# Performance work log

Hardware: AMD Instinct MI355X
Metric: run time of the kernel (lower is better)

Reference implementation:

```python
import jax, jax.numpy as jnp
import numpy as np

B, T, C = 2, 2048, 1024
H = 16
HD = C // H  # 64
SCALE = 0.1 / (HD ** 0.5)


def setup_inputs() -> dict:
    key = jax.random.key(0)
    k1, k2, k3 = jax.random.split(key, 3)
    x = jax.random.normal(k1, (B, T, C), dtype=jnp.float32)
    W_attn = jax.random.normal(k2, (C, 3 * C), dtype=jnp.float32) * (C ** -0.5)
    b_attn = jnp.zeros((3 * C,), dtype=jnp.float32)
    W_proj = jax.random.normal(k3, (C, C), dtype=jnp.float32) * (C ** -0.5)
    b_proj = jnp.zeros((C,), dtype=jnp.float32)
    return {"x": x, "W_attn": W_attn, "b_attn": b_attn, "W_proj": W_proj, "b_proj": b_proj}


def reference(x, W_attn, b_attn, W_proj, b_proj):
    Bx, Tx, Cx = x.shape
    qkv = x @ W_attn + b_attn  # [B,T,3C]
    q, k, v = jnp.split(qkv, 3, axis=-1)
    # [B,T,C] -> [B,H,T,HD]
    q = q.reshape(Bx, Tx, H, HD).transpose(0, 2, 1, 3)
    k = k.reshape(Bx, Tx, H, HD).transpose(0, 2, 1, 3)
    v = v.reshape(Bx, Tx, H, HD).transpose(0, 2, 1, 3)
    # note the extra 0.1 factor baked into this module's scaling
    attn = jnp.einsum('bhqd,bhkd->bhqk', q, k) * SCALE
    causal = jnp.tril(jnp.ones((Tx, Tx), dtype=bool))
    attn = jnp.where(causal[None, None, :, :], attn, -jnp.inf)
    attn = jax.nn.softmax(attn, axis=-1)
    y = jnp.einsum('bhqk,bhkd->bhqd', attn, v)
    y = y.transpose(0, 2, 1, 3).reshape(Bx, Tx, Cx)
    return y @ W_proj + b_proj
```

## Files before the change

kernel.cpp:

```cpp
#include <hip/hip_runtime.h>

typedef unsigned short u16;
typedef unsigned int u32;
typedef float f32x4 __attribute__((ext_vector_type(4)));
typedef float f32x16 __attribute__((ext_vector_type(16)));
typedef __bf16 bf16x8 __attribute__((ext_vector_type(8)));
typedef u16 u16x8 __attribute__((ext_vector_type(8)));
typedef u32 u32x4 __attribute__((ext_vector_type(4)));

#define ATT_SCALE 0.0125f
#define LOG2E 1.4426950408889634f

__device__ __forceinline__ u16 f2bf(float x) {
  unsigned u = __builtin_bit_cast(unsigned, x);
  u += 0x7fffu + ((u >> 16) & 1u);
  return (u16)(u >> 16);
}

__device__ __forceinline__ u32 pack_bf16(float lo, float hi) {
  __bf16 a = (__bf16)lo, b = (__bf16)hi;
  return ((u32)__builtin_bit_cast(u16, b) << 16) | __builtin_bit_cast(u16, a);
}

__device__ __forceinline__ float fexp2(float x) {
  return __builtin_amdgcn_exp2f(x);
}

__device__ __forceinline__ f32x4 mfma16(u16x8 a, u16x8 b, f32x4 c) {
  return __builtin_amdgcn_mfma_f32_16x16x32_bf16(
      __builtin_bit_cast(bf16x8, a), __builtin_bit_cast(bf16x8, b), c, 0, 0, 0);
}

__device__ __forceinline__ f32x16 mfma32(u16x8 a, u16x8 b, f32x16 c) {
  return __builtin_amdgcn_mfma_f32_32x32x16_bf16(
      __builtin_bit_cast(bf16x8, a), __builtin_bit_cast(bf16x8, b), c, 0, 0, 0);
}

__device__ __forceinline__ void gl_lds16(const void* g, void* l) {
  __builtin_amdgcn_global_load_lds(
      (__attribute__((address_space(1))) void*)g,
      (__attribute__((address_space(3))) void*)l, 16, 0, 0);
}

__global__ void k_pre(const float* __restrict__ x, const float* __restrict__ W_attn,
                      const float* __restrict__ W_proj, u16* __restrict__ x_bf,
                      u16* __restrict__ Wt_a, u16* __restrict__ Wt_p) {
  __shared__ float tile[32][33];
  const int id = blockIdx.x, tid = threadIdx.x;
  if (id < 2048) {
    int base = id * 2048 + tid * 4;
#pragma unroll
    for (int s = 0; s < 2; ++s) {
      int i = base + s * 1024;
      float4 v = *(const float4*)&x[i];
      ushort4 o;
      o.x = f2bf(v.x); o.y = f2bf(v.y); o.z = f2bf(v.z); o.w = f2bf(v.w);
      *(ushort4*)&x_bf[i] = o;
    }
    return;
  }
  const float* in;
  u16* outp;
  int rows, cols, bx, by;
  if (id < 5120) {
    int t2 = id - 2048;
    bx = t2 % 96; by = t2 / 96;
    in = W_attn; outp = Wt_a; rows = 1024; cols = 3072;
  } else {
    int t3 = id - 5120;
    bx = t3 & 31; by = t3 >> 5;
    in = W_proj; outp = Wt_p; rows = 1024; cols = 1024;
  }
  int tx = tid & 31, ty = tid >> 5;
  int n0 = bx * 32, k0 = by * 32;
#pragma unroll
  for (int i = 0; i < 32; i += 8)
    tile[ty + i][tx] = in[(size_t)(k0 + ty + i) * cols + n0 + tx];
  __syncthreads();
#pragma unroll
  for (int i = 0; i < 32; i += 8)
    outp[(size_t)(n0 + ty + i) * rows + k0 + tx] = f2bf(tile[tx][ty + i]);
}

__global__ void k_gemm_qkv(const u16* __restrict__ A, const u16* __restrict__ Bt,
                           const float* __restrict__ bias,
                           u16* __restrict__ qb, u16* __restrict__ kb, u16* __restrict__ vTb) {
  __shared__ u16 Al[128 * 64];
  __shared__ u16 Bl[128 * 64];
  const int tid = threadIdx.x;
  const int lane = tid & 63;
  const int w = tid >> 6;
  const int m0 = blockIdx.y * 128;
  const int n0 = blockIdx.x * 128;
  const int wr = (w >> 1) * 64;
  const int wc = (w & 1) * 64;
  const int lr = lane & 15;
  const int lk = (lane >> 4) * 8;

  f32x4 acc[4][4] = {};

  for (int k0 = 0; k0 < 1024; k0 += 64) {
#pragma unroll
    for (int it = 0; it < 4; ++it) {
      int off = (it * 256 + tid) * 8;
      int r = off >> 6, c = off & 63;
      gl_lds16(&A[(size_t)(m0 + r) * 1024 + k0 + c], &Al[off]);
      gl_lds16(&Bt[(size_t)(n0 + r) * 1024 + k0 + c], &Bl[off]);
    }
    __syncthreads();
#pragma unroll
    for (int kk = 0; kk < 64; kk += 32) {
      u16x8 af[4], bf[4];
#pragma unroll
      for (int i = 0; i < 4; ++i) {
        af[i] = *(const u16x8*)&Al[(wr + i * 16 + lr) * 64 + kk + lk];
        bf[i] = *(const u16x8*)&Bl[(wc + i * 16 + lr) * 64 + kk + lk];
      }
#pragma unroll
      for (int i = 0; i < 4; ++i)
#pragma unroll
        for (int j = 0; j < 4; ++j)
          acc[i][j] = mfma16(af[i], bf[j], acc[i][j]);
    }
    __syncthreads();
  }

#pragma unroll
  for (int i = 0; i < 4; ++i) {
    int rowb = m0 + wr + i * 16 + ((lane >> 4) << 2);
#pragma unroll
    for (int j = 0; j < 4; ++j) {
      int col = n0 + wc + j * 16 + lr;
      float bv = bias[col];
      int which = col >> 10;
      int c = col & 1023;
      int h = c >> 6, d = c & 63;
      int b_ = rowb >> 11, t0 = rowb & 2047;
      int bh = b_ * 16 + h;
      if (which == 2) {
        ushort4 st;
        st.x = f2bf(acc[i][j][0] + bv);
        st.y = f2bf(acc[i][j][1] + bv);
        st.z = f2bf(acc[i][j][2] + bv);
        st.w = f2bf(acc[i][j][3] + bv);
        *(ushort4*)&vTb[((size_t)bh * 64 + d) * 2048 + t0] = st;
      } else {
        u16* dst = (which == 0) ? qb : kb;
        float sc = (which == 0) ? (ATT_SCALE * LOG2E) : 1.0f;
#pragma unroll
        for (int r = 0; r < 4; ++r) {
          float fv = (acc[i][j][r] + bv) * sc;
          dst[((size_t)bh * 2048 + t0 + r) * 64 + d] = f2bf(fv);
        }
      }
    }
  }
}

__device__ __forceinline__ void stage_pair(const u16* __restrict__ kb_bh,
                                           const u16* __restrict__ vT_bh,
                                           u16* Kd, u16* Vd, int kv0, int tid) {
#pragma unroll
  for (int it = 0; it < 4; ++it) {
    int ch = it * 256 + tid;
    int r = ch >> 3, c = ch & 7;
    gl_lds16(&kb_bh[(size_t)(kv0 + r) * 64 + (c ^ (r & 7)) * 8], &Kd[ch * 8]);
    int r2 = ch >> 4, c2 = ch & 15;
    int h2 = c2 >> 3, cc = c2 & 7;
    gl_lds16(&vT_bh[(size_t)r2 * 2048 + kv0 + (h2 * 8 + (cc ^ (r2 & 7))) * 8],
             &Vd[ch * 8]);
  }
}

__global__ __launch_bounds__(256) void k_attn(const u16* __restrict__ qb,
                                              const u16* __restrict__ kb,
                                              const u16* __restrict__ vTb,
                                              u16* __restrict__ yb) {
  __shared__ u16 Kl[2][8192];
  __shared__ u16 Vl[2][8192];

  const int tid = threadIdx.x, lane = tid & 63, w = tid >> 6;
  const int wq = w & 1;
  const int wp = w >> 1;
  const int id = blockIdx.x;
  const int bh = (id & 7) + ((id >> 7) << 3);
  const int pairi = (id >> 3) & 15;
  const int b_ = bh >> 4, h = bh & 15;
  const int ql = lane & 31;
  const int hi = lane >> 5;

  const u16* kb_bh = kb + (size_t)bh * 2048 * 64;
  const u16* vT_bh = vTb + (size_t)bh * 64 * 2048;

#pragma unroll 1
  for (int phase = 0; phase < 2; ++phase) {
    const int qt = phase ? (31 - pairi) : pairi;
    const int q0w = qt * 64 + wq * 32;
    const int qg = q0w + ql;
    const int lim = wq * 32 + ql;

    const u16* qrow = qb + ((size_t)bh * 2048 + qg) * 64;
    u16x8 qf[4];
#pragma unroll
    for (int ks = 0; ks < 4; ++ks)
      qf[ks] = *(const u16x8*)&qrow[ks * 16 + hi * 8];

    f32x16 o0 = {}, o1 = {};
    float mrow = -1e30f, lrow = 0.f;

    const int nkv = qt + 1;
    const int niter = (nkv + 1) >> 1;
    stage_pair(kb_bh, vT_bh, Kl[0], Vl[0], 0, tid);
    int cur = 0;

#pragma unroll 1
    for (int it = 0; it < niter; ++it) {
      if (it + 1 < niter) {
        stage_pair(kb_bh, vT_bh, Kl[cur ^ 1], Vl[cur ^ 1], (it + 1) * 128, tid);
        asm volatile("s_waitcnt vmcnt(8)" ::: "memory");
      } else {
        asm volatile("s_waitcnt vmcnt(0)" ::: "memory");
      }
      __builtin_amdgcn_sched_barrier(0);
      __builtin_amdgcn_s_barrier();

      const int mytile = 2 * it + wp;
      if (mytile <= qt) {
        const u16* Kc = Kl[cur];
        const u16* Vc = Vl[cur];
        const int rbase = wp * 64;

        f32x16 s0 = {}, s1 = {};
        __builtin_amdgcn_s_setprio(1);
#pragma unroll
        for (int ks = 0; ks < 4; ++ks) {
          int ch = 2 * ks + hi;
          int r0 = rbase + ql, r1 = rbase + 32 + ql;
          u16x8 kf0 = *(const u16x8*)&Kc[r0 * 64 + ((ch ^ (r0 & 7)) * 8)];
          u16x8 kf1 = *(const u16x8*)&Kc[r1 * 64 + ((ch ^ (r1 & 7)) * 8)];
          s0 = mfma32(kf0, qf[ks], s0);
          s1 = mfma32(kf1, qf[ks], s1);
        }
        __builtin_amdgcn_s_setprio(0);

        const bool diag = (mytile == qt);
        float pv[32];
        float tmax = -1e30f;
#pragma unroll
        for (int r = 0; r < 16; ++r) {
          float a = s0[r], b2 = s1[r];
          if (diag) {
            int kl0 = (r & 3) + 8 * (r >> 2) + 4 * hi;
            if (kl0 > lim) a = -1e30f;
            if (kl0 + 32 > lim) b2 = -1e30f;
          }
          pv[r] = a;
          pv[16 + r] = b2;
          tmax = fmaxf(tmax, fmaxf(a, b2));
        }
        float rmax = fmaxf(tmax, __shfl_xor(tmax, 32, 64));

        if (__any(rmax > mrow + 8.0f)) {
          float mn = fmaxf(mrow, rmax);
          float al = fexp2(mrow - mn);
          mrow = mn;
          lrow *= al;
#pragma unroll
          for (int r = 0; r < 16; ++r) { o0[r] *= al; o1[r] *= al; }
        }

        u32 pw[16];
#pragma unroll
        for (int j = 0; j < 16; ++j) {
          float e0 = fexp2(pv[2 * j] - mrow);
          float e1 = fexp2(pv[2 * j + 1] - mrow);
          lrow += e0 + e1;
          pw[j] = pack_bf16(e0, e1);
        }

#pragma unroll
        for (int tt = 0; tt < 2; ++tt)
#pragma unroll
          for (int u = 0; u < 2; ++u)
#pragma unroll
            for (int z = 0; z < 2; ++z) {
              int jA = tt * 8 + u * 4 + z;
              asm volatile("v_permlane32_swap_b32 %0, %1"
                           : "+v"(pw[jA]), "+v"(pw[jA + 2]));
            }

        __builtin_amdgcn_s_setprio(1);
#pragma unroll
        for (int ks = 0; ks < 4; ++ks) {
          u32x4 pwv = {pw[4 * ks], pw[4 * ks + 1], pw[4 * ks + 2], pw[4 * ks + 3]};
          u16x8 pfrag = __builtin_bit_cast(u16x8, pwv);
          int ch = 2 * ks + hi;
          int rv0 = ql, rv1 = 32 + ql;
          u16x8 vf0 = *(const u16x8*)&Vc[rv0 * 128 + (wp * 8 + (ch ^ (rv0 & 7))) * 8];
          u16x8 vf1 = *(const u16x8*)&Vc[rv1 * 128 + (wp * 8 + (ch ^ (rv1 & 7))) * 8];
          o0 = mfma32(vf0, pfrag, o0);
          o1 = mfma32(vf1, pfrag, o1);
        }
        __builtin_amdgcn_s_setprio(0);
      }
      __builtin_amdgcn_s_barrier();
      cur ^= 1;
    }

    __syncthreads();
    float* mb = (float*)&Kl[0][0];
    if (wp == 1) {
      float4* dst = (float4*)&mb[(wq * 64 + lane) * 37];
      float4 hd; hd.x = mrow; hd.y = lrow; hd.z = 0.f; hd.w = 0.f;
      dst[0] = hd;
#pragma unroll
      for (int j = 0; j < 4; ++j) {
        float4 t0 = {o0[4 * j], o0[4 * j + 1], o0[4 * j + 2], o0[4 * j + 3]};
        float4 t1 = {o1[4 * j], o1[4 * j + 1], o1[4 * j + 2], o1[4 * j + 3]};
        dst[1 + j] = t0;
        dst[5 + j] = t1;
      }
    }
    __syncthreads();
    if (wp == 0) {
      const float4* src = (const float4*)&mb[(wq * 64 + lane) * 37];
      float4 hd = src[0];
      float m2 = hd.x, l2 = hd.y;
      float m = fmaxf(mrow, m2);
      float a1 = fexp2(mrow - m), a2 = fexp2(m2 - m);
      float l = lrow * a1 + l2 * a2;
      l += __shfl_xor(l, 32, 64);
      float inv = 1.0f / l;

      size_t ybase = ((size_t)b_ * 2048 + qg) * 1024 + h * 64;
#pragma unroll
      for (int dt = 0; dt < 2; ++dt) {
#pragma unroll
        for (int rg = 0; rg < 4; ++rg) {
          float4 po = src[1 + dt * 4 + rg];
          const f32x16& ov = dt ? o1 : o0;
          int d0 = dt * 32 + 8 * rg + 4 * hi;
          ushort4 st;
          st.x = f2bf((ov[rg * 4 + 0] * a1 + po.x * a2) * inv);
          st.y = f2bf((ov[rg * 4 + 1] * a1 + po.y * a2) * inv);
          st.z = f2bf((ov[rg * 4 + 2] * a1 + po.z * a2) * inv);
          st.w = f2bf((ov[rg * 4 + 3] * a1 + po.w * a2) * inv);
          *(ushort4*)&yb[ybase + d0] = st;
        }
      }
    }
    __syncthreads();
  }
}

__global__ void k_gemm_out(const u16* __restrict__ A, const u16* __restrict__ Bt,
                           const float* __restrict__ bias, float* __restrict__ out) {
  __shared__ u16 Al[64 * 64];
  __shared__ u16 Bl[128 * 64];
  const int tid = threadIdx.x;
  const int lane = tid & 63;
  const int w = tid >> 6;
  const int m0 = blockIdx.y * 64;
  const int n0 = blockIdx.x * 128;
  const int wr = (w >> 1) * 32;
  const int wc = (w & 1) * 64;
  const int lr = lane & 15;
  const int lk = (lane >> 4) * 8;

  f32x4 acc[2][4] = {};

  for (int k0 = 0; k0 < 1024; k0 += 64) {
#pragma unroll
    for (int it = 0; it < 2; ++it) {
      int ch = it * 256 + tid;
      int r = ch >> 3, c = (ch & 7) * 8;
      gl_lds16(&A[(size_t)(m0 + r) * 1024 + k0 + c], &Al[ch * 8]);
    }
#pragma unroll
    for (int it = 0; it < 4; ++it) {
      int ch = it * 256 + tid;
      int r = ch >> 3, c = (ch & 7) * 8;
      gl_lds16(&Bt[(size_t)(n0 + r) * 1024 + k0 + c], &Bl[ch * 8]);
    }
    __syncthreads();
#pragma unroll
    for (int kk = 0; kk < 64; kk += 32) {
      u16x8 af[2], bf[4];
#pragma unroll
      for (int i = 0; i < 2; ++i)
        af[i] = *(const u16x8*)&Al[(wr + i * 16 + lr) * 64 + kk + lk];
#pragma unroll
      for (int j = 0; j < 4; ++j)
        bf[j] = *(const u16x8*)&Bl[(wc + j * 16 + lr) * 64 + kk + lk];
#pragma unroll
      for (int i = 0; i < 2; ++i)
#pragma unroll
        for (int j = 0; j < 4; ++j)
          acc[i][j] = mfma16(af[i], bf[j], acc[i][j]);
    }
    __syncthreads();
  }

#pragma unroll
  for (int i = 0; i < 2; ++i) {
    int rowb = m0 + wr + i * 16 + ((lane >> 4) << 2);
#pragma unroll
    for (int j = 0; j < 4; ++j) {
      int col = n0 + wc + j * 16 + lr;
      float bv = bias[col];
#pragma unroll
      for (int r = 0; r < 4; ++r)
        out[(size_t)(rowb + r) * 1024 + col] = acc[i][j][r] + bv;
    }
  }
}

extern "C" void kernel_launch(void* const* d_in, const int* in_sizes, int n_in,
                              void* d_out, int out_size, void* d_ws, size_t ws_size,
                              hipStream_t stream) {
  const float* x      = (const float*)d_in[0];
  const float* W_attn = (const float*)d_in[1];
  const float* b_attn = (const float*)d_in[2];
  const float* W_proj = (const float*)d_in[3];
  const float* b_proj = (const float*)d_in[4];
  float* out = (float*)d_out;

  char* ws = (char*)d_ws;
  const size_t MB = 1024 * 1024;
  u16* x_bf  = (u16*)(ws);
  u16* Wt_a  = (u16*)(ws + 8 * MB);
  u16* Wt_p  = (u16*)(ws + 14 * MB);
  u16* qbf   = (u16*)(ws + 16 * MB);
  u16* kbf   = (u16*)(ws + 24 * MB);
  u16* vTbf  = (u16*)(ws + 32 * MB);
  u16* ybf   = (u16*)(ws + 40 * MB);

  k_pre<<<6144, 256, 0, stream>>>(x, W_attn, W_proj, x_bf, Wt_a, Wt_p);
  k_gemm_qkv<<<dim3(24, 32), 256, 0, stream>>>(x_bf, Wt_a, b_attn, qbf, kbf, vTbf);
  k_attn<<<512, 256, 0, stream>>>(qbf, kbf, vTbf, ybf);
  k_gemm_out<<<dim3(8, 64), 256, 0, stream>>>(ybf, Wt_p, b_proj, out);
}
```

Before: 112.3 us.

## Rewrite QKV GEMM with 256x256 tiles, double-buffered swizzled LDS, and priority hints

The QKV projection GEMM moves from 128x128 tiles on 256 threads to 256x256 tiles on 512 threads. Global-to-LDS loads for the next k-step are double-buffered and overlapped with MFMA work using explicit vmcnt waits and barriers. An XOR swizzle is added to the LDS layout to avoid bank conflicts, and setprio is raised around the MFMA bursts. The larger tiles improve data reuse, but the grid shrinks to 192 blocks, which may leave some of the 256 CUs idle and raises register pressure from 32 accumulators per thread.

Result: slower. 124.6 us (+10.9%).

```diff
diff --git a/kernel.cpp b/kernel.cpp
--- a/kernel.cpp
+++ b/kernel.cpp
@@ -82,74 +82,114 @@
     outp[(size_t)(n0 + ty + i) * rows + k0 + tx] = f2bf(tile[tx][ty + i]);
 }
 
-__global__ void k_gemm_qkv(const u16* __restrict__ A, const u16* __restrict__ Bt,
-                           const float* __restrict__ bias,
-                           u16* __restrict__ qb, u16* __restrict__ kb, u16* __restrict__ vTb) {
-  __shared__ u16 Al[128 * 64];
-  __shared__ u16 Bl[128 * 64];
-  const int tid = threadIdx.x;
-  const int lane = tid & 63;
-  const int w = tid >> 6;
-  const int m0 = blockIdx.y * 128;
-  const int n0 = blockIdx.x * 128;
-  const int wr = (w >> 1) * 64;
-  const int wc = (w & 1) * 64;
+__global__ __launch_bounds__(512) void k_gemm_qkv(const u16* __restrict__ A,
+                                                  const u16* __restrict__ Bt,
+                                                  const float* __restrict__ bias,
+                                                  u16* __restrict__ qb,
+                                                  u16* __restrict__ kb,
+                                                  u16* __restrict__ vTb) {
+  __shared__ u16 AL[2][2][256 * 32];
+  __shared__ u16 BL[2][2][256 * 32];
+  const int tid = threadIdx.x, lane = tid & 63, w = tid >> 6;
+  const int wr = w >> 2;
+  const int wc = w & 3;
+  const int m0 = blockIdx.y * 256;
+  const int n0 = blockIdx.x * 256;
   const int lr = lane & 15;
-  const int lk = (lane >> 4) * 8;
-
-  f32x4 acc[4][4] = {};
-
-  for (int k0 = 0; k0 < 1024; k0 += 64) {
-#pragma unroll
-    for (int it = 0; it < 4; ++it) {
-      int off = (it * 256 + tid) * 8;
-      int r = off >> 6, c = off & 63;
-      gl_lds16(&A[(size_t)(m0 + r) * 1024 + k0 + c], &Al[off]);
-      gl_lds16(&Bt[(size_t)(n0 + r) * 1024 + k0 + c], &Bl[off]);
-    }
-    __syncthreads();
-#pragma unroll
-    for (int kk = 0; kk < 64; kk += 32) {
-      u16x8 af[4], bf[4];
-#pragma unroll
-      for (int i = 0; i < 4; ++i) {
-        af[i] = *(const u16x8*)&Al[(wr + i * 16 + lr) * 64 + kk + lk];
-        bf[i] = *(const u16x8*)&Bl[(wc + i * 16 + lr) * 64 + kk + lk];
-      }
-#pragma unroll
-      for (int i = 0; i < 4; ++i)
-#pragma unroll
-        for (int j = 0; j < 4; ++j)
-          acc[i][j] = mfma16(af[i], bf[j], acc[i][j]);
-    }
-    __syncthreads();
-  }
-
-#pragma unroll
-  for (int i = 0; i < 4; ++i) {
-    int rowb = m0 + wr + i * 16 + ((lane >> 4) << 2);
-#pragma unroll
-    for (int j = 0; j < 4; ++j) {
-      int col = n0 + wc + j * 16 + lr;
+  const int lg = lane >> 4;
+
+  f32x4 acc[8][4] = {};
+
+#define STAGE_UNIT(SRC, DST, nb, p, kt)                                        \
+  {                                                                            \
+    _Pragma("unroll") for (int it_ = 0; it_ < 2; ++it_) {                      \
+      int ch = it_ * 512 + tid;                  \
+      int r_ = ch >> 2, c_ = ch & 3;                                           \
+      gl_lds16(&SRC[(size_t)((m0n0_##SRC) + r_) * 1024 + (kt) * 64 +           \
+                    (p) * 32 + ((c_ ^ (r_ & 3)) * 8)],                         \
+               &DST[nb][p][ch * 8]);                                           \
+    }                                                                          \
+  }
+  const int m0n0_A = m0;
+  const int m0n0_Bt = n0;
+
+  STAGE_UNIT(A, AL, 0, 0, 0);
+  STAGE_UNIT(Bt, BL, 0, 0, 0);
+  STAGE_UNIT(A, AL, 0, 1, 0);
+  STAGE_UNIT(Bt, BL, 0, 1, 0);
+  int cur = 0;
+
+#pragma unroll 1
+  for (int t = 0; t < 16; ++t) {
+#pragma unroll
+    for (int p = 0; p < 2; ++p) {
+      if (t + 1 < 16) {
+        STAGE_UNIT(A, AL, cur ^ 1, p, t + 1);
+        STAGE_UNIT(Bt, BL, cur ^ 1, p, t + 1);
+        asm volatile("s_waitcnt vmcnt(8)" ::: "memory");
+      } else if (p == 0) {
+        asm volatile("s_waitcnt vmcnt(4)" ::: "memory");
+      } else {
+        asm volatile("s_waitcnt vmcnt(0)" ::: "memory");
+      }
+      __builtin_amdgcn_sched_barrier(0);
+      __builtin_amdgcn_s_barrier();
+
+      u16x8 bf[4];
+#pragma unroll
+      for (int nj = 0; nj < 4; ++nj) {
+        int rb = wc * 64 + nj * 16 + lr;
+        bf[nj] = *(const u16x8*)&BL[cur][p][rb * 32 + ((lg ^ (rb & 3)) * 8)];
+      }
+#pragma unroll
+      for (int mh = 0; mh < 2; ++mh) {
+        u16x8 af[4];
+#pragma unroll
+        for (int q = 0; q < 4; ++q) {
+          int mi = mh * 4 + q;
+          int ra = wr * 128 + mi * 16 + lr;
+          af[q] = *(const u16x8*)&AL[cur][p][ra * 32 + ((lg ^ (ra & 3)) * 8)];
+        }
+        __builtin_amdgcn_s_setprio(1);
+#pragma unroll
+        for (int q = 0; q < 4; ++q)
+#pragma unroll
+          for (int nj = 0; nj < 4; ++nj)
+            acc[mh * 4 + q][nj] = mfma16(af[q], bf[nj], acc[mh * 4 + q][nj]);
+        __builtin_amdgcn_s_setprio(0);
+      }
+      __builtin_amdgcn_s_barrier();
+    }
+    cur ^= 1;
+  }
+#undef STAGE_UNIT
+
+  const int which = n0 >> 10;
+  const int b_ = m0 >> 11;
+#pragma unroll
+  for (int mi = 0; mi < 8; ++mi) {
+    int row = m0 + wr * 128 + mi * 16 + lg * 4;
+    int t0 = row & 2047;
+#pragma unroll
+    for (int nj = 0; nj < 4; ++nj) {
+      int col = n0 + wc * 64 + nj * 16 + lr;
       float bv = bias[col];
-      int which = col >> 10;
       int c = col & 1023;
       int h = c >> 6, d = c & 63;
-      int b_ = rowb >> 11, t0 = rowb & 2047;
       int bh = b_ * 16 + h;
       if (which == 2) {
         ushort4 st;
-        st.x = f2bf(acc[i][j][0] + bv);
-        st.y = f2bf(acc[i][j][1] + bv);
-        st.z = f2bf(acc[i][j][2] + bv);
-        st.w = f2bf(acc[i][j][3] + bv);
+        st.x = f2bf(acc[mi][nj][0] + bv);
+        st.y = f2bf(acc[mi][nj][1] + bv);
+        st.z = f2bf(acc[mi][nj][2] + bv);
+        st.w = f2bf(acc[mi][nj][3] + bv);
         *(ushort4*)&vTb[((size_t)bh * 64 + d) * 2048 + t0] = st;
       } else {
         u16* dst = (which == 0) ? qb : kb;
         float sc = (which == 0) ? (ATT_SCALE * LOG2E) : 1.0f;
 #pragma unroll
         for (int r = 0; r < 4; ++r) {
-          float fv = (acc[i][j][r] + bv) * sc;
+          float fv = (acc[mi][nj][r] + bv) * sc;
           dst[((size_t)bh * 2048 + t0 + r) * 64 + d] = f2bf(fv);
         }
       }
@@ -436,7 +476,7 @@
   u16* ybf   = (u16*)(ws + 40 * MB);
 
   k_pre<<<6144, 256, 0, stream>>>(x, W_attn, W_proj, x_bf, Wt_a, Wt_p);
-  k_gemm_qkv<<<dim3(24, 32), 256, 0, stream>>>(x_bf, Wt_a, b_attn, qbf, kbf, vTbf);
+  k_gemm_qkv<<<dim3(12, 16), 512, 0, stream>>>(x_bf, Wt_a, b_attn, qbf, kbf, vTbf);
   k_attn<<<512, 256, 0, stream>>>(qbf, kbf, vTbf, ybf);
   k_gemm_out<<<dim3(8, 64), 256, 0, stream>>>(ybf, Wt_p, b_proj, out);
 }
```
